# Performance work log

Hardware: AMD Instinct MI355X
Metric: run time of the kernel (lower is better)

## Reference

```python
import jax, jax.numpy as jnp
import numpy as np

SCALES = (128, 128, 128)  # (Dx, Dy, Dz)

# 8 corner offsets of the trilinear cell, (8, 3)
_OFFSETS = np.array([[(i >> 2) & 1, (i >> 1) & 1, i & 1] for i in range(8)], dtype=np.float32)


def _gridding(pts, scales):
    """Trilinear point splatting (scatter-add) into a flattened 3D voxel grid.

    pts: (B, N, 3) in [-1, 1]. Returns (B, Dx*Dy*Dz).
    Mirrors GRNet's gridding_distance.forward: points scaled by scale/2,
    grid vertices span [-scale//2, scale//2 - 1] per dim.
    """
    Dx, Dy, Dz = scales
    mins = jnp.array([-(Dx // 2), -(Dy // 2), -(Dz // 2)], dtype=pts.dtype)
    scale_factors = jnp.array([Dx / 2.0, Dy / 2.0, Dz / 2.0], dtype=pts.dtype)

    p = pts * scale_factors                     # (B, N, 3), scaled coords
    lower = jnp.floor(p)                        # lower corner per dim
    frac = p - lower                            # fractional offset in [0,1)

    offs = jnp.asarray(_OFFSETS, dtype=pts.dtype)            # (8, 3)
    # trilinear weights: prod over dims of frac (upper) or 1-frac (lower)
    w = jnp.prod(
        jnp.where(offs[None, None] > 0, frac[:, :, None, :], 1.0 - frac[:, :, None, :]),
        axis=-1,
    )                                                          # (B, N, 8)

    idx = (lower[:, :, None, :] + offs[None, None]) - mins     # (B, N, 8, 3)
    idx = idx.astype(jnp.int32)
    dims = jnp.array([Dx, Dy, Dz], dtype=jnp.int32)
    valid = jnp.all((idx >= 0) & (idx < dims), axis=-1)        # (B, N, 8)

    flat = (idx[..., 0] * Dy + idx[..., 1]) * Dz + idx[..., 2]  # (B, N, 8)
    flat = jnp.where(valid, flat, 0)
    w = jnp.where(valid, w, jnp.zeros((), pts.dtype))

    n_verts = Dx * Dy * Dz

    def scatter_one(f, wt):
        return jnp.zeros((n_verts,), pts.dtype).at[f.reshape(-1)].add(wt.reshape(-1))

    return jax.vmap(scatter_one)(flat, w)       # (B, n_verts)


def setup_inputs() -> dict:
    key = jax.random.key(0)
    k1, k2 = jax.random.split(key)
    B, N = 4, 262144
    # uniform in [-0.98, 0.98] so all 8 trilinear corners stay in-grid
    pred_cloud = jax.random.uniform(k1, (B, N, 3), dtype=jnp.float32, minval=-0.98, maxval=0.98)
    gt_cloud = jax.random.uniform(k2, (B, N, 3), dtype=jnp.float32, minval=-0.98, maxval=0.98)
    return {"pred_cloud": pred_cloud, "gt_cloud": gt_cloud}


def reference(pred_cloud, gt_cloud):
    pred_grid = _gridding(pred_cloud, SCALES)
    gt_grid = _gridding(gt_cloud, SCALES)
    return pred_grid, gt_grid
```

## Files before the change

### kernel.cpp

```cpp
#include <hip/hip_runtime.h>

#define DXYZ 128
#define NVERT (DXYZ * DXYZ * DXYZ)
#define SBINS 128
#define RX 8
#define RY 16
#define CHUNK 2048
#define PTHREADS 512
#define PPT (CHUNK / PTHREADS)
#define GTHREADS 1024
#define FIX 16777216.0f
#define INVFIX (1.0f / 16777216.0f)

typedef float nf4 __attribute__((ext_vector_type(4)));


__global__ __launch_bounds__(PTHREADS, 8) void scatter_onepass(
    const float* __restrict__ p0, const float* __restrict__ p1,
    unsigned* __restrict__ gcnt,
    uint2* __restrict__ sorted,
    int N, int B, int nchunks, unsigned capacity)
{
    __shared__ unsigned h[SBINS];
    __shared__ unsigned cur[SBINS];

    const int blk = blockIdx.x;
    const int tid = threadIdx.x;
    const int cb = blk / nchunks;
    const int c  = blk - cb * nchunks;
    const float* p = (cb < B ? p0 : p1) +
                     ((size_t)(cb % B) * N + (size_t)c * CHUNK) * 3;

    if (tid < SBINS) h[tid] = 0u;
    __syncthreads();

    unsigned rlo[PPT], rezi[PPT], rxy[PPT];
#pragma unroll
    for (int j = 0; j < PPT; ++j) {
        int i = tid + j * PTHREADS;
        float px = p[3*i+0] * 64.0f;
        float py = p[3*i+1] * 64.0f;
        float pz = p[3*i+2] * 64.0f;
        float lx = floorf(px), ly = floorf(py), lz = floorf(pz);
        int ix = (int)lx + 64, iy = (int)ly + 64, iz = (int)lz + 64;
        unsigned ex = min((unsigned)((px - lx) * 65536.0f), 65535u);
        unsigned ey = min((unsigned)((py - ly) * 65536.0f), 65535u);
        unsigned ez = min((unsigned)((pz - lz) * 65536.0f), 65535u);
        rlo[j]  = ex | (ey << 16);
        rezi[j] = ez | ((unsigned)iz << 16);
        rxy[j]  = (unsigned)ix | ((unsigned)iy << 16);
        int bx0 = ix >> 3, by0 = iy >> 4;
        int bx1 = (ix+1) >> 3, by1 = (iy+1) >> 4;
        for (int bx = bx0; bx <= bx1; ++bx)
            for (int by = by0; by <= by1; ++by)
                atomicAdd(&h[(bx << 3) + by], 1u);
    }
    __syncthreads();

    if (tid < SBINS)
        cur[tid] = atomicAdd(&gcnt[cb * SBINS + tid], h[tid]);
    __syncthreads();

    size_t sbase = (size_t)cb * SBINS * capacity;
#pragma unroll
    for (int j = 0; j < PPT; ++j) {
        unsigned lo = rlo[j];
        unsigned ez = rezi[j] & 0xffffu;
        unsigned iz = rezi[j] >> 16;
        int ix = (int)(rxy[j] & 0xffffu);
        int iy = (int)(rxy[j] >> 16);
        int bx0 = ix >> 3, by0 = iy >> 4;
        int bx1 = (ix+1) >> 3, by1 = (iy+1) >> 4;
        for (int bx = bx0; bx <= bx1; ++bx)
            for (int by = by0; by <= by1; ++by) {
                unsigned llx = (unsigned)(ix - (bx << 3) + 1);
                unsigned lly = (unsigned)(iy - (by << 4) + 1);
                unsigned hi = ez | (llx << 16) | (lly << 20) | (iz << 25);
                int k = (bx << 3) + by;
                unsigned slot = atomicAdd(&cur[k], 1u);
                if (slot < capacity)
                    sorted[sbase + (size_t)k * capacity + slot] =
                        make_uint2(lo, hi);
            }
    }
}

__global__ __launch_bounds__(GTHREADS, 8) void gather3_kernel(
    const uint2* __restrict__ sorted,
    const unsigned* __restrict__ gcnt,
    float* __restrict__ out, unsigned capacity)
{
    __shared__ unsigned acc[RX * RY * DXYZ];
    const int g = blockIdx.x;
    const int tid = threadIdx.x;
    const int cb = g >> 7;
    const int r = g & (SBINS - 1);
    const int rx = r >> 3, ry = r & 7;
    const int x0 = rx << 3, y0 = ry << 4;

    uint4* a4 = (uint4*)acc;
    uint4 z4 = make_uint4(0u, 0u, 0u, 0u);
    for (int i = tid; i < RX * RY * DXYZ / 4; i += GTHREADS) a4[i] = z4;
    __syncthreads();

    const float inv = 1.0f / 65536.0f;
    unsigned cnt = min(gcnt[g], capacity);
    size_t s = (size_t)g * capacity;
    for (unsigned i = tid; i < cnt; i += GTHREADS) {
        uint2 rec = sorted[s + i];
        float fx = (float)(rec.x & 0xffffu) * inv;
        float fy = (float)(rec.x >> 16) * inv;
        float fz = (float)(rec.y & 0xffffu) * inv;
        int lx = (int)((rec.y >> 16) & 15u) - 1;
        int ly = (int)((rec.y >> 20) & 31u) - 1;
        int zc = (int)(rec.y >> 25);
        float gx[2] = {1.0f - fx, fx};
        float gy[2] = {1.0f - fy, fy};
        float gz[2] = {1.0f - fz, fz};
#pragma unroll
        for (int dx = 0; dx < 2; ++dx) {
            int cx = lx + dx;
            if ((unsigned)cx >= (unsigned)RX) continue;
#pragma unroll
            for (int dy = 0; dy < 2; ++dy) {
                int cy = ly + dy;
                if ((unsigned)cy >= (unsigned)RY) continue;
#pragma unroll
                for (int dz = 0; dz < 2; ++dz) {
                    int cz = zc + dz;
                    if ((unsigned)cz >= (unsigned)DXYZ) continue;
                    unsigned w = (unsigned)(gx[dx] * gy[dy] * gz[dz]
                                            * FIX + 0.5f);
                    atomicAdd(&acc[((cx << 4) + cy) * DXYZ + cz], w);
                }
            }
        }
    }
    __syncthreads();

    float* ob = out + (size_t)cb * NVERT;
    for (int i = tid; i < RX * RY * DXYZ / 4; i += GTHREADS) {
        int cx = i >> 9;
        int t = i & 511;
        size_t base = (((size_t)(x0 + cx) * DXYZ) + (size_t)y0) * DXYZ;
        nf4* dst = (nf4*)(ob + base);
        const uint4* src = (const uint4*)&acc[cx * (RY * DXYZ)];
        uint4 u = src[t];
        nf4 f = {(float)u.x * INVFIX, (float)u.y * INVFIX,
                 (float)u.z * INVFIX, (float)u.w * INVFIX};
        __builtin_nontemporal_store(f, &dst[t]);
    }
}

__global__ __launch_bounds__(256) void splat_kernel(
    const float* __restrict__ pts, float* __restrict__ out,
    int n_per_batch, int total)
{
    int t = blockIdx.x * blockDim.x + threadIdx.x;
    if (t >= total) return;
    float px = pts[3*t+0] * 64.0f, py = pts[3*t+1] * 64.0f, pz = pts[3*t+2] * 64.0f;
    float lx = floorf(px), ly = floorf(py), lz = floorf(pz);
    float fx = px - lx, fy = py - ly, fz = pz - lz;
    int ix = (int)lx + 64, iy = (int)ly + 64, iz = (int)lz + 64;
    int b = t / n_per_batch;
    float* o = out + (size_t)b * NVERT;
    size_t base = ((size_t)ix * DXYZ + (size_t)iy) * DXYZ + (size_t)iz;
    float gx[2] = {1.0f-fx, fx}, gy[2] = {1.0f-fy, fy}, gz[2] = {1.0f-fz, fz};
#pragma unroll
    for (int dx = 0; dx < 2; ++dx)
#pragma unroll
        for (int dy = 0; dy < 2; ++dy)
#pragma unroll
            for (int dz = 0; dz < 2; ++dz)
                atomicAdd(o + base + (size_t)dx * (DXYZ*DXYZ) + dy * DXYZ + dz,
                          gx[dx] * gy[dy] * gz[dz]);
}

static inline size_t align256(size_t x) { return (x + 255) & ~(size_t)255; }

extern "C" void kernel_launch(void* const* d_in, const int* in_sizes, int n_in,
                              void* d_out, int out_size, void* d_ws, size_t ws_size,
                              hipStream_t stream) {
    const float* pred = (const float*)d_in[0];
    const float* gt   = (const float*)d_in[1];
    float* out = (float*)d_out;

    int total = in_sizes[0] / 3;
    int B = out_size / (2 * NVERT);
    int N = total / B;
    int CB = 2 * B;
    int nchunks = N / CHUNK;
    int nkeys = CB * SBINS;
    int nblocks = CB * nchunks;
    bool divisible = (N % CHUNK) == 0 && N > 0;

    unsigned mean = (unsigned)(((size_t)N * 5 / 4) / SBINS);
    unsigned capacity = ((mean * 2) + 255u) & ~255u;
    if (capacity < 1024u) capacity = 1024u;

    size_t off_gcnt   = 0;
    size_t off_sorted = align256((size_t)nkeys * 4);
    size_t need = off_sorted + (size_t)nkeys * capacity * sizeof(uint2);

    if (!divisible || ws_size < need) {
        (void)hipMemsetAsync(d_out, 0, (size_t)out_size * sizeof(float), stream);
        int blocks = (total + 255) / 256;
        splat_kernel<<<blocks, 256, 0, stream>>>(pred, out, N, total);
        splat_kernel<<<blocks, 256, 0, stream>>>(gt, out + (size_t)B * NVERT, N, total);
        return;
    }

    char* ws = (char*)d_ws;
    unsigned* gcnt = (unsigned*)(ws + off_gcnt);
    uint2*    sorted = (uint2*)(ws + off_sorted);

    (void)hipMemsetAsync(gcnt, 0, (size_t)nkeys * 4, stream);
    scatter_onepass<<<nblocks, PTHREADS, 0, stream>>>(pred, gt, gcnt, sorted,
                                                      N, B, nchunks, capacity);
    gather3_kernel<<<nkeys, GTHREADS, 0, stream>>>(sorted, gcnt, out, capacity);
}
```

Before: 112.4 us.

## Stage per-chunk bin records in shared memory and write fixed-size segments

Replaces the global atomic bin counters with per-chunk shared-memory staging: each scatter block bins its points into fixed 60-slot LDS sub-buckets, then writes them as coalesced uint4 segments along with per-segment counts. The gather kernel walks all chunk segments for its bin and skips empty slots. Input loads are vectorized as float4. This removes the global atomics and the memset, but pads global traffic to full segment capacity, uses much more LDS (lower occupancy), and silently drops records if a bin exceeds 60 per chunk.

```diff
diff --git a/kernel.cpp b/kernel.cpp
--- a/kernel.cpp
+++ b/kernel.cpp
@@ -7,21 +7,21 @@
 #define RY 16
 #define CHUNK 2048
 #define PTHREADS 512
-#define PPT (CHUNK / PTHREADS)
 #define GTHREADS 1024
+#define SUBCAP 60
 #define FIX 16777216.0f
 #define INVFIX (1.0f / 16777216.0f)
 
 typedef float nf4 __attribute__((ext_vector_type(4)));
 
 
-__global__ __launch_bounds__(PTHREADS, 8) void scatter_onepass(
+__global__ __launch_bounds__(PTHREADS, 4) void scatter_stage(
     const float* __restrict__ p0, const float* __restrict__ p1,
-    unsigned* __restrict__ gcnt,
     uint2* __restrict__ sorted,
-    int N, int B, int nchunks, unsigned capacity)
+    unsigned* __restrict__ cnts,
+    int N, int B, int nchunks)
 {
-    __shared__ unsigned h[SBINS];
+    __shared__ __align__(16) uint2 stage[SBINS * SUBCAP];
     __shared__ unsigned cur[SBINS];
 
     const int blk = blockIdx.x;
@@ -31,64 +31,62 @@
     const float* p = (cb < B ? p0 : p1) +
                      ((size_t)(cb % B) * N + (size_t)c * CHUNK) * 3;
 
-    if (tid < SBINS) h[tid] = 0u;
-    __syncthreads();
-
-    unsigned rlo[PPT], rezi[PPT], rxy[PPT];
-#pragma unroll
-    for (int j = 0; j < PPT; ++j) {
-        int i = tid + j * PTHREADS;
-        float px = p[3*i+0] * 64.0f;
-        float py = p[3*i+1] * 64.0f;
-        float pz = p[3*i+2] * 64.0f;
+    if (tid < SBINS) cur[tid] = 0u;
+    __syncthreads();
+
+    const float4* pv = (const float4*)p;
+    float4 f0 = pv[3 * tid + 0];
+    float4 f1 = pv[3 * tid + 1];
+    float4 f2 = pv[3 * tid + 2];
+    float xs[4] = {f0.x, f0.w, f1.z, f2.y};
+    float ys[4] = {f0.y, f1.x, f1.w, f2.z};
+    float zs[4] = {f0.z, f1.y, f2.x, f2.w};
+
+#pragma unroll
+    for (int j = 0; j < 4; ++j) {
+        float px = xs[j] * 64.0f;
+        float py = ys[j] * 64.0f;
+        float pz = zs[j] * 64.0f;
         float lx = floorf(px), ly = floorf(py), lz = floorf(pz);
         int ix = (int)lx + 64, iy = (int)ly + 64, iz = (int)lz + 64;
         unsigned ex = min((unsigned)((px - lx) * 65536.0f), 65535u);
         unsigned ey = min((unsigned)((py - ly) * 65536.0f), 65535u);
         unsigned ez = min((unsigned)((pz - lz) * 65536.0f), 65535u);
-        rlo[j]  = ex | (ey << 16);
-        rezi[j] = ez | ((unsigned)iz << 16);
-        rxy[j]  = (unsigned)ix | ((unsigned)iy << 16);
+        unsigned lo = ex | (ey << 16);
         int bx0 = ix >> 3, by0 = iy >> 4;
-        int bx1 = (ix+1) >> 3, by1 = (iy+1) >> 4;
-        for (int bx = bx0; bx <= bx1; ++bx)
-            for (int by = by0; by <= by1; ++by)
-                atomicAdd(&h[(bx << 3) + by], 1u);
-    }
-    __syncthreads();
-
-    if (tid < SBINS)
-        cur[tid] = atomicAdd(&gcnt[cb * SBINS + tid], h[tid]);
-    __syncthreads();
-
-    size_t sbase = (size_t)cb * SBINS * capacity;
-#pragma unroll
-    for (int j = 0; j < PPT; ++j) {
-        unsigned lo = rlo[j];
-        unsigned ez = rezi[j] & 0xffffu;
-        unsigned iz = rezi[j] >> 16;
-        int ix = (int)(rxy[j] & 0xffffu);
-        int iy = (int)(rxy[j] >> 16);
-        int bx0 = ix >> 3, by0 = iy >> 4;
-        int bx1 = (ix+1) >> 3, by1 = (iy+1) >> 4;
+        int bx1 = (ix + 1) >> 3, by1 = (iy + 1) >> 4;
         for (int bx = bx0; bx <= bx1; ++bx)
             for (int by = by0; by <= by1; ++by) {
                 unsigned llx = (unsigned)(ix - (bx << 3) + 1);
                 unsigned lly = (unsigned)(iy - (by << 4) + 1);
-                unsigned hi = ez | (llx << 16) | (lly << 20) | (iz << 25);
+                unsigned hi = ez | (llx << 16) | (lly << 20) |
+                              ((unsigned)iz << 25);
                 int k = (bx << 3) + by;
                 unsigned slot = atomicAdd(&cur[k], 1u);
-                if (slot < capacity)
-                    sorted[sbase + (size_t)k * capacity + slot] =
-                        make_uint2(lo, hi);
+                if (slot < SUBCAP)
+                    stage[k * SUBCAP + slot] = make_uint2(lo, hi);
             }
     }
-}
-
-__global__ __launch_bounds__(GTHREADS, 8) void gather3_kernel(
+    __syncthreads();
+
+    const uint4* s4 = (const uint4*)stage;
+    size_t segbase = (size_t)cb * SBINS * (size_t)nchunks + (size_t)c;
+    for (int j = tid; j < SBINS * (SUBCAP / 2); j += PTHREADS) {
+        int k = j / (SUBCAP / 2);
+        int r = j - k * (SUBCAP / 2);
+        size_t segIdx = segbase + (size_t)k * nchunks;
+        ((uint4*)(sorted + segIdx * SUBCAP))[r] = s4[j];
+    }
+    if (tid < SBINS) {
+        size_t segIdx = segbase + (size_t)tid * nchunks;
+        cnts[segIdx] = min(cur[tid], (unsigned)SUBCAP);
+    }
+}
+
+__global__ __launch_bounds__(GTHREADS, 8) void gather_kernel(
     const uint2* __restrict__ sorted,
-    const unsigned* __restrict__ gcnt,
-    float* __restrict__ out, unsigned capacity)
+    const unsigned* __restrict__ cnts,
+    float* __restrict__ out, int nchunks)
 {
     __shared__ unsigned acc[RX * RY * DXYZ];
     const int g = blockIdx.x;
@@ -104,34 +102,41 @@
     __syncthreads();
 
     const float inv = 1.0f / 65536.0f;
-    unsigned cnt = min(gcnt[g], capacity);
-    size_t s = (size_t)g * capacity;
-    for (unsigned i = tid; i < cnt; i += GTHREADS) {
-        uint2 rec = sorted[s + i];
-        float fx = (float)(rec.x & 0xffffu) * inv;
-        float fy = (float)(rec.x >> 16) * inv;
-        float fz = (float)(rec.y & 0xffffu) * inv;
-        int lx = (int)((rec.y >> 16) & 15u) - 1;
-        int ly = (int)((rec.y >> 20) & 31u) - 1;
-        int zc = (int)(rec.y >> 25);
-        float gx[2] = {1.0f - fx, fx};
-        float gy[2] = {1.0f - fy, fy};
-        float gz[2] = {1.0f - fz, fz};
-#pragma unroll
-        for (int dx = 0; dx < 2; ++dx) {
-            int cx = lx + dx;
-            if ((unsigned)cx >= (unsigned)RX) continue;
-#pragma unroll
-            for (int dy = 0; dy < 2; ++dy) {
-                int cy = ly + dy;
-                if ((unsigned)cy >= (unsigned)RY) continue;
-#pragma unroll
-                for (int dz = 0; dz < 2; ++dz) {
-                    int cz = zc + dz;
-                    if ((unsigned)cz >= (unsigned)DXYZ) continue;
-                    unsigned w = (unsigned)(gx[dx] * gy[dy] * gz[dz]
-                                            * FIX + 0.5f);
-                    atomicAdd(&acc[((cx << 4) + cy) * DXYZ + cz], w);
+    const int slots = nchunks * SUBCAP;
+    size_t keybase = (size_t)g * (size_t)nchunks;
+    const uint2* srec = sorted + keybase * SUBCAP;
+    const unsigned* kcnt = cnts + keybase;
+
+    for (int s = tid; s < slots; s += GTHREADS) {
+        int c = s / SUBCAP;
+        int idx = s - c * SUBCAP;
+        if ((unsigned)idx < kcnt[c]) {
+            uint2 rec = srec[s];
+            float fx = (float)(rec.x & 0xffffu) * inv;
+            float fy = (float)(rec.x >> 16) * inv;
+            float fz = (float)(rec.y & 0xffffu) * inv;
+            int lx = (int)((rec.y >> 16) & 15u) - 1;
+            int ly = (int)((rec.y >> 20) & 31u) - 1;
+            int zc = (int)(rec.y >> 25);
+            float gx[2] = {1.0f - fx, fx};
+            float gy[2] = {1.0f - fy, fy};
+            float gz[2] = {1.0f - fz, fz};
+#pragma unroll
+            for (int dx = 0; dx < 2; ++dx) {
+                int cx = lx + dx;
+                if ((unsigned)cx >= (unsigned)RX) continue;
+#pragma unroll
+                for (int dy = 0; dy < 2; ++dy) {
+                    int cy = ly + dy;
+                    if ((unsigned)cy >= (unsigned)RY) continue;
+#pragma unroll
+                    for (int dz = 0; dz < 2; ++dz) {
+                        int cz = zc + dz;
+                        if ((unsigned)cz >= (unsigned)DXYZ) continue;
+                        unsigned w = (unsigned)(gx[dx] * gy[dy] * gz[dz]
+                                                * FIX + 0.5f);
+                        atomicAdd(&acc[((cx << 4) + cy) * DXYZ + cz], w);
+                    }
                 }
             }
         }
@@ -194,13 +199,10 @@
     int nblocks = CB * nchunks;
     bool divisible = (N % CHUNK) == 0 && N > 0;
 
-    unsigned mean = (unsigned)(((size_t)N * 5 / 4) / SBINS);
-    unsigned capacity = ((mean * 2) + 255u) & ~255u;
-    if (capacity < 1024u) capacity = 1024u;
-
-    size_t off_gcnt   = 0;
-    size_t off_sorted = align256((size_t)nkeys * 4);
-    size_t need = off_sorted + (size_t)nkeys * capacity * sizeof(uint2);
+    size_t nseg = (size_t)nkeys * (size_t)nchunks;
+    size_t off_sorted = 0;
+    size_t off_cnts = align256(nseg * SUBCAP * sizeof(uint2));
+    size_t need = off_cnts + nseg * 4;
 
     if (!divisible || ws_size < need) {
         (void)hipMemsetAsync(d_out, 0, (size_t)out_size * sizeof(float), stream);
@@ -211,11 +213,10 @@
     }
 
     char* ws = (char*)d_ws;
-    unsigned* gcnt = (unsigned*)(ws + off_gcnt);
     uint2*    sorted = (uint2*)(ws + off_sorted);
-
-    (void)hipMemsetAsync(gcnt, 0, (size_t)nkeys * 4, stream);
-    scatter_onepass<<<nblocks, PTHREADS, 0, stream>>>(pred, gt, gcnt, sorted,
-                                                      N, B, nchunks, capacity);
-    gather3_kernel<<<nkeys, GTHREADS, 0, stream>>>(sorted, gcnt, out, capacity);
-}
+    unsigned* cnts   = (unsigned*)(ws + off_cnts);
+
+    scatter_stage<<<nblocks, PTHREADS, 0, stream>>>(pred, gt, sorted, cnts,
+                                                    N, B, nchunks);
+    gather_kernel<<<nkeys, GTHREADS, 0, stream>>>(sorted, cnts, out, nchunks);
+}
```

Result: slower. 119.6 us (+6.4%).

## Fuse scatter and gather into persistent kernel with grid-wide barrier

Applied to the files above, without the earlier changes.

Replaces the two-kernel scatter/gather pipeline with one persistent kernel of 512 blocks. Each block loops over point chunks, then all blocks meet at a software device barrier, and each block then accumulates region tiles in shared memory. Point loads become float4 vector reads. The goal is to drop a kernel launch and the tail at the kernel boundary. In exchange the gather phase runs with 512 threads per block and few resident blocks, so parallelism and latency hiding drop, and the spin barrier assumes all 512 blocks are co-resident.

```diff
diff --git a/kernel.cpp b/kernel.cpp
--- a/kernel.cpp
+++ b/kernel.cpp
@@ -8,6 +8,7 @@
 #define CHUNK 2048
 #define PTHREADS 512
 #define PPT (CHUNK / PTHREADS)
+#define FBLOCKS 512
 #define GTHREADS 1024
 #define FIX 16777216.0f
 #define INVFIX (1.0f / 16777216.0f)
@@ -15,15 +16,180 @@
 typedef float nf4 __attribute__((ext_vector_type(4)));
 
 
+__device__ __forceinline__ void device_barrier(unsigned* bar, unsigned nblk) {
+    __syncthreads();
+    if (threadIdx.x == 0) {
+        __threadfence();
+        unsigned a = __hip_atomic_fetch_add(&bar[0], 1u, __ATOMIC_ACQ_REL,
+                                            __HIP_MEMORY_SCOPE_AGENT);
+        if (a + 1u == nblk) {
+            __hip_atomic_store(&bar[1], 1u, __ATOMIC_RELEASE,
+                               __HIP_MEMORY_SCOPE_AGENT);
+        } else {
+            while (__hip_atomic_load(&bar[1], __ATOMIC_ACQUIRE,
+                                     __HIP_MEMORY_SCOPE_AGENT) == 0u)
+                __builtin_amdgcn_s_sleep(8);
+        }
+        __threadfence();
+    }
+    __syncthreads();
+}
+
+__global__ __launch_bounds__(PTHREADS, 4) void fused_kernel(
+    const float* __restrict__ p0, const float* __restrict__ p1,
+    unsigned* __restrict__ gcnt,
+    unsigned* __restrict__ bar,
+    uint2* __restrict__ sorted,
+    float* __restrict__ out,
+    int N, int B, int nchunks, int nkeys, unsigned capacity)
+{
+    __shared__ __align__(16) unsigned acc[RX * RY * DXYZ];
+    const int tid = threadIdx.x;
+    const int g = blockIdx.x;
+    const int ntasks = 2 * B * nchunks;
+
+    unsigned* h   = acc;
+    unsigned* cur = acc + SBINS;
+
+    for (int task = g; task < ntasks; task += FBLOCKS) {
+        const int cb = task / nchunks;
+        const int c  = task - cb * nchunks;
+        const float* p = (cb < B ? p0 : p1) +
+                         ((size_t)(cb % B) * N + (size_t)c * CHUNK) * 3;
+
+        if (tid < SBINS) h[tid] = 0u;
+        __syncthreads();
+
+        const float4* pv = (const float4*)p;
+        float4 f0 = pv[3 * tid + 0];
+        float4 f1 = pv[3 * tid + 1];
+        float4 f2 = pv[3 * tid + 2];
+        float xs[4] = {f0.x, f0.w, f1.z, f2.y};
+        float ys[4] = {f0.y, f1.x, f1.w, f2.z};
+        float zs[4] = {f0.z, f1.y, f2.x, f2.w};
+
+        unsigned rlo[PPT], rezi[PPT], rxy[PPT];
+#pragma unroll
+        for (int j = 0; j < PPT; ++j) {
+            float px = xs[j] * 64.0f;
+            float py = ys[j] * 64.0f;
+            float pz = zs[j] * 64.0f;
+            float lx = floorf(px), ly = floorf(py), lz = floorf(pz);
+            int ix = (int)lx + 64, iy = (int)ly + 64, iz = (int)lz + 64;
+            unsigned ex = min((unsigned)((px - lx) * 65536.0f), 65535u);
+            unsigned ey = min((unsigned)((py - ly) * 65536.0f), 65535u);
+            unsigned ez = min((unsigned)((pz - lz) * 65536.0f), 65535u);
+            rlo[j]  = ex | (ey << 16);
+            rezi[j] = ez | ((unsigned)iz << 16);
+            rxy[j]  = (unsigned)ix | ((unsigned)iy << 16);
+            int bx0 = ix >> 3, by0 = iy >> 4;
+            int bx1 = (ix + 1) >> 3, by1 = (iy + 1) >> 4;
+            for (int bx = bx0; bx <= bx1; ++bx)
+                for (int by = by0; by <= by1; ++by)
+                    atomicAdd(&h[(bx << 3) + by], 1u);
+        }
+        __syncthreads();
+
+        if (tid < SBINS)
+            cur[tid] = atomicAdd(&gcnt[cb * SBINS + tid], h[tid]);
+        __syncthreads();
+
+        size_t sbase = (size_t)cb * SBINS * capacity;
+#pragma unroll
+        for (int j = 0; j < PPT; ++j) {
+            unsigned lo = rlo[j];
+            unsigned ez = rezi[j] & 0xffffu;
+            unsigned iz = rezi[j] >> 16;
+            int ix = (int)(rxy[j] & 0xffffu);
+            int iy = (int)(rxy[j] >> 16);
+            int bx0 = ix >> 3, by0 = iy >> 4;
+            int bx1 = (ix + 1) >> 3, by1 = (iy + 1) >> 4;
+            for (int bx = bx0; bx <= bx1; ++bx)
+                for (int by = by0; by <= by1; ++by) {
+                    unsigned llx = (unsigned)(ix - (bx << 3) + 1);
+                    unsigned lly = (unsigned)(iy - (by << 4) + 1);
+                    unsigned hi = ez | (llx << 16) | (lly << 20) | (iz << 25);
+                    int k = (bx << 3) + by;
+                    unsigned slot = atomicAdd(&cur[k], 1u);
+                    if (slot < capacity)
+                        sorted[sbase + (size_t)k * capacity + slot] =
+                            make_uint2(lo, hi);
+                }
+        }
+        __syncthreads();
+    }
+
+    device_barrier(bar, (unsigned)FBLOCKS);
+
+    const float inv = 1.0f / 65536.0f;
+    for (int key = g; key < nkeys; key += FBLOCKS) {
+        const int cb = key >> 7;
+        const int r = key & (SBINS - 1);
+        const int rx = r >> 3, ry = r & 7;
+        const int x0 = rx << 3, y0 = ry << 4;
+
+        uint4* a4 = (uint4*)acc;
+        uint4 z4 = make_uint4(0u, 0u, 0u, 0u);
+        for (int i = tid; i < RX * RY * DXYZ / 4; i += PTHREADS) a4[i] = z4;
+        __syncthreads();
+
+        unsigned cnt = min(gcnt[key], capacity);
+        size_t s = (size_t)key * capacity;
+        for (unsigned i = tid; i < cnt; i += PTHREADS) {
+            uint2 rec = sorted[s + i];
+            float fx = (float)(rec.x & 0xffffu) * inv;
+            float fy = (float)(rec.x >> 16) * inv;
+            float fz = (float)(rec.y & 0xffffu) * inv;
+            int lx = (int)((rec.y >> 16) & 15u) - 1;
+            int ly = (int)((rec.y >> 20) & 31u) - 1;
+            int zc = (int)(rec.y >> 25);
+            float gx[2] = {1.0f - fx, fx};
+            float gy[2] = {1.0f - fy, fy};
+            float gz[2] = {1.0f - fz, fz};
+#pragma unroll
+            for (int dx = 0; dx < 2; ++dx) {
+                int cx = lx + dx;
+                if ((unsigned)cx >= (unsigned)RX) continue;
+#pragma unroll
+                for (int dy = 0; dy < 2; ++dy) {
+                    int cy = ly + dy;
+                    if ((unsigned)cy >= (unsigned)RY) continue;
+#pragma unroll
+                    for (int dz = 0; dz < 2; ++dz) {
+                        int cz = zc + dz;
+                        if ((unsigned)cz >= (unsigned)DXYZ) continue;
+                        unsigned w = (unsigned)(gx[dx] * gy[dy] * gz[dz]
+                                                * FIX + 0.5f);
+                        atomicAdd(&acc[((cx << 4) + cy) * DXYZ + cz], w);
+                    }
+                }
+            }
+        }
+        __syncthreads();
+
+        float* ob = out + (size_t)cb * NVERT;
+        for (int i = tid; i < RX * RY * DXYZ / 4; i += PTHREADS) {
+            int cx = i >> 9;
+            int t = i & 511;
+            size_t base = (((size_t)(x0 + cx) * DXYZ) + (size_t)y0) * DXYZ;
+            nf4* dst = (nf4*)(ob + base);
+            const uint4* src = (const uint4*)&acc[cx * (RY * DXYZ)];
+            uint4 u = src[t];
+            nf4 f = {(float)u.x * INVFIX, (float)u.y * INVFIX,
+                     (float)u.z * INVFIX, (float)u.w * INVFIX};
+            __builtin_nontemporal_store(f, &dst[t]);
+        }
+        __syncthreads();
+    }
+}
+
 __global__ __launch_bounds__(PTHREADS, 8) void scatter_onepass(
     const float* __restrict__ p0, const float* __restrict__ p1,
-    unsigned* __restrict__ gcnt,
-    uint2* __restrict__ sorted,
+    unsigned* __restrict__ gcnt, uint2* __restrict__ sorted,
     int N, int B, int nchunks, unsigned capacity)
 {
     __shared__ unsigned h[SBINS];
     __shared__ unsigned cur[SBINS];
-
     const int blk = blockIdx.x;
     const int tid = threadIdx.x;
     const int cb = blk / nchunks;
@@ -34,10 +200,24 @@
     if (tid < SBINS) h[tid] = 0u;
     __syncthreads();
 
-    unsigned rlo[PPT], rezi[PPT], rxy[PPT];
-#pragma unroll
-    for (int j = 0; j < PPT; ++j) {
-        int i = tid + j * PTHREADS;
+    for (int i = tid; i < CHUNK; i += PTHREADS) {
+        float px = p[3*i+0] * 64.0f;
+        float py = p[3*i+1] * 64.0f;
+        int ix = (int)floorf(px) + 64;
+        int iy = (int)floorf(py) + 64;
+        int bx0 = ix >> 3, by0 = iy >> 4;
+        int bx1 = (ix+1) >> 3, by1 = (iy+1) >> 4;
+        for (int bx = bx0; bx <= bx1; ++bx)
+            for (int by = by0; by <= by1; ++by)
+                atomicAdd(&h[(bx << 3) + by], 1u);
+    }
+    __syncthreads();
+
+    if (tid < SBINS)
+        cur[tid] = atomicAdd(&gcnt[cb * SBINS + tid], h[tid]);
+    __syncthreads();
+
+    for (int i = tid; i < CHUNK; i += PTHREADS) {
         float px = p[3*i+0] * 64.0f;
         float py = p[3*i+1] * 64.0f;
         float pz = p[3*i+2] * 64.0f;
@@ -46,48 +226,26 @@
         unsigned ex = min((unsigned)((px - lx) * 65536.0f), 65535u);
         unsigned ey = min((unsigned)((py - ly) * 65536.0f), 65535u);
         unsigned ez = min((unsigned)((pz - lz) * 65536.0f), 65535u);
-        rlo[j]  = ex | (ey << 16);
-        rezi[j] = ez | ((unsigned)iz << 16);
-        rxy[j]  = (unsigned)ix | ((unsigned)iy << 16);
-        int bx0 = ix >> 3, by0 = iy >> 4;
-        int bx1 = (ix+1) >> 3, by1 = (iy+1) >> 4;
-        for (int bx = bx0; bx <= bx1; ++bx)
-            for (int by = by0; by <= by1; ++by)
-                atomicAdd(&h[(bx << 3) + by], 1u);
-    }
-    __syncthreads();
-
-    if (tid < SBINS)
-        cur[tid] = atomicAdd(&gcnt[cb * SBINS + tid], h[tid]);
-    __syncthreads();
-
-    size_t sbase = (size_t)cb * SBINS * capacity;
-#pragma unroll
-    for (int j = 0; j < PPT; ++j) {
-        unsigned lo = rlo[j];
-        unsigned ez = rezi[j] & 0xffffu;
-        unsigned iz = rezi[j] >> 16;
-        int ix = (int)(rxy[j] & 0xffffu);
-        int iy = (int)(rxy[j] >> 16);
+        unsigned lo = ex | (ey << 16);
         int bx0 = ix >> 3, by0 = iy >> 4;
         int bx1 = (ix+1) >> 3, by1 = (iy+1) >> 4;
         for (int bx = bx0; bx <= bx1; ++bx)
             for (int by = by0; by <= by1; ++by) {
                 unsigned llx = (unsigned)(ix - (bx << 3) + 1);
                 unsigned lly = (unsigned)(iy - (by << 4) + 1);
-                unsigned hi = ez | (llx << 16) | (lly << 20) | (iz << 25);
+                unsigned hi = ez | (llx << 16) | (lly << 20) |
+                              ((unsigned)iz << 25);
                 int k = (bx << 3) + by;
                 unsigned slot = atomicAdd(&cur[k], 1u);
                 if (slot < capacity)
-                    sorted[sbase + (size_t)k * capacity + slot] =
+                    sorted[(size_t)(cb * SBINS + k) * capacity + slot] =
                         make_uint2(lo, hi);
             }
     }
 }
 
 __global__ __launch_bounds__(GTHREADS, 8) void gather3_kernel(
-    const uint2* __restrict__ sorted,
-    const unsigned* __restrict__ gcnt,
+    const uint2* __restrict__ sorted, const unsigned* __restrict__ gcnt,
     float* __restrict__ out, unsigned capacity)
 {
     __shared__ unsigned acc[RX * RY * DXYZ];
@@ -191,7 +349,7 @@
     int CB = 2 * B;
     int nchunks = N / CHUNK;
     int nkeys = CB * SBINS;
-    int nblocks = CB * nchunks;
+    int ntasks = CB * nchunks;
     bool divisible = (N % CHUNK) == 0 && N > 0;
 
     unsigned mean = (unsigned)(((size_t)N * 5 / 4) / SBINS);
@@ -199,7 +357,8 @@
     if (capacity < 1024u) capacity = 1024u;
 
     size_t off_gcnt   = 0;
-    size_t off_sorted = align256((size_t)nkeys * 4);
+    size_t off_bar    = align256((size_t)nkeys * 4);
+    size_t off_sorted = off_bar + 256;
     size_t need = off_sorted + (size_t)nkeys * capacity * sizeof(uint2);
 
     if (!divisible || ws_size < need) {
@@ -211,11 +370,19 @@
     }
 
     char* ws = (char*)d_ws;
-    unsigned* gcnt = (unsigned*)(ws + off_gcnt);
+    unsigned* gcnt   = (unsigned*)(ws + off_gcnt);
+    unsigned* bar    = (unsigned*)(ws + off_bar);
     uint2*    sorted = (uint2*)(ws + off_sorted);
 
-    (void)hipMemsetAsync(gcnt, 0, (size_t)nkeys * 4, stream);
-    scatter_onepass<<<nblocks, PTHREADS, 0, stream>>>(pred, gt, gcnt, sorted,
-                                                      N, B, nchunks, capacity);
+    (void)hipMemsetAsync(ws, 0, off_sorted, stream);
+
+    if (ntasks % FBLOCKS == 0 && nkeys % FBLOCKS == 0 && ntasks >= FBLOCKS) {
+        fused_kernel<<<FBLOCKS, PTHREADS, 0, stream>>>(
+            pred, gt, gcnt, bar, sorted, out, N, B, nchunks, nkeys, capacity);
+        return;
+    }
+
+    scatter_onepass<<<ntasks, PTHREADS, 0, stream>>>(pred, gt, gcnt, sorted,
+                                                     N, B, nchunks, capacity);
     gather3_kernel<<<nkeys, GTHREADS, 0, stream>>>(sorted, gcnt, out, capacity);
 }
```

Result: slower. 237.4 us (+111.2%).
